# Performance work log

Hardware: AMD Instinct MI355X
Metric: run time of the kernel (lower is better)

Reference implementation:

```python
import jax, jax.numpy as jnp
import numpy as np

NUM_HEADS = 8
NUM_LAYERS = 6
NUM_POINTS = 25
# TrajParamIndex: X=0,Y=1,Z=2,VX=3,VY=4,AX=5,AY=6,YAW=7,LENGTH=8,WIDTH=9,HEIGHT=10


def _unit_cube_points(n=NUM_POINTS):
    m = int(np.sqrt(n))
    lin = np.linspace(-1.0, 1.0, m)
    pts = []
    for dim in range(3):
        for sign in (-1.0, 1.0):
            a, b = np.meshgrid(lin, lin, indexing='ij')
            s = np.full_like(a, sign)
            if dim == 0:
                p = np.stack([s, a, b], -1)
            elif dim == 1:
                p = np.stack([a, s, b], -1)
            else:
                p = np.stack([a, b, s], -1)
            pts.append(p.reshape(-1, 3))
    return jnp.asarray(np.concatenate(pts, 0), jnp.float32)  # [150,3]


def _ln(x, g, b):
    m = x.mean(-1, keepdims=True)
    v = ((x - m) ** 2).mean(-1, keepdims=True)
    return (x - m) / jnp.sqrt(v + 1e-5) * g + b


def _mha(q, k, v, wi, bi, wo, bo):
    E = q.shape[-1]
    d = E // NUM_HEADS
    qq = q @ wi[:E].T + bi[:E]
    kk = k @ wi[E:2 * E].T + bi[E:2 * E]
    vv = v @ wi[2 * E:].T + bi[2 * E:]
    B, S, _ = qq.shape
    Sk = kk.shape[1]
    qh = qq.reshape(B, S, NUM_HEADS, d)
    kh = kk.reshape(B, Sk, NUM_HEADS, d)
    vh = vv.reshape(B, Sk, NUM_HEADS, d)
    att = jnp.einsum('bqhd,bkhd->bhqk', qh, kh) / jnp.sqrt(jnp.float32(d))
    att = jax.nn.softmax(att, axis=-1)
    o = jnp.einsum('bhqk,bkhd->bqhd', att, vh).reshape(B, S, E)
    return o @ wo.T + bo


def _bilinear(feat, uv, valid):
    # feat [B,C,H,W], uv [B,M,2] in [0,1] (u along W), valid [B,M] -> [B,M,C]
    B, C, H, W = feat.shape
    px = uv[..., 0] * (W - 1)
    py = uv[..., 1] * (H - 1)
    x0 = jnp.floor(px)
    y0 = jnp.floor(py)
    wx = px - x0
    wy = py - y0
    x0i = jnp.clip(x0, 0, W - 1).astype(jnp.int32)
    x1i = jnp.clip(x0 + 1, 0, W - 1).astype(jnp.int32)
    y0i = jnp.clip(y0, 0, H - 1).astype(jnp.int32)
    y1i = jnp.clip(y0 + 1, 0, H - 1).astype(jnp.int32)
    flat = feat.reshape(B, C, H * W)
    take = jax.vmap(lambda f, i: f[:, i])  # [C,HW],[M] -> [C,M]
    f00 = take(flat, y0i * W + x0i)
    f01 = take(flat, y0i * W + x1i)
    f10 = take(flat, y1i * W + x0i)
    f11 = take(flat, y1i * W + x1i)
    wxb = wx[:, None, :]
    wyb = wy[:, None, :]
    out = (f00 * (1 - wxb) * (1 - wyb) + f01 * wxb * (1 - wyb)
           + f10 * (1 - wxb) * wyb + f11 * wxb * wyb)
    out = out * valid[:, None, :].astype(out.dtype)
    return out.transpose(0, 2, 1)


def _transform_points(box_pts, tp, ego_t, dt):
    # box_pts [B,N,P,3] local, tp [B,N,11], ego_t [B,4] (x,y,yaw,ts), dt [B]
    yaw = tp[..., 7][..., None]  # [B,N,1]
    c, s = jnp.cos(yaw), jnp.sin(yaw)
    lx, ly, lz = box_pts[..., 0], box_pts[..., 1], box_pts[..., 2]
    rx = lx * c - ly * s
    ry = lx * s + ly * c
    dtb = dt[:, None]  # [B,1]
    cx = tp[..., 0] + tp[..., 3] * dtb + 0.5 * tp[..., 5] * dtb ** 2  # [B,N]
    cy = tp[..., 1] + tp[..., 4] * dtb + 0.5 * tp[..., 6] * dtb ** 2
    cz = tp[..., 2]
    wx = rx + cx[..., None]
    wy = ry + cy[..., None]
    wz = lz + cz[..., None]
    ex = ego_t[:, 0][:, None, None]
    ey = ego_t[:, 1][:, None, None]
    eyaw = ego_t[:, 2][:, None, None]
    pxr = wx - ex
    pyr = wy - ey
    gx = pxr * jnp.cos(eyaw) + pyr * jnp.sin(eyaw)
    gy = -pxr * jnp.sin(eyaw) + pyr * jnp.cos(eyaw)
    return jnp.stack([gx, gy, wz], -1)


def _project(wp, cal):
    # wp [B,N,P,3], cal [B,8] = fx,fy,cx,cy,tx,ty,tz,cam_yaw -> uv in [0,1], valid
    fx, fy, cx0, cy0, tx, ty, tz, cyaw = [cal[:, i][:, None, None] for i in range(8)]
    px = wp[..., 0] - tx
    py = wp[..., 1] - ty
    pz = wp[..., 2] - tz
    fwd = px * jnp.cos(cyaw) + py * jnp.sin(cyaw)
    left = -px * jnp.sin(cyaw) + py * jnp.cos(cyaw)
    zc = fwd
    xc = -left
    yc = -pz
    vz = zc > 0.1
    zs = jnp.maximum(zc, 0.1)
    u = fx * xc / zs + cx0
    v = fy * yc / zs + cy0
    valid = vz & (u >= 0) & (u < 1) & (v >= 0) & (v < 1)
    return jnp.stack([u, v], -1), valid


def _forward(features, calib, ego_states, queries, query_pos,
             traj_w1, traj_b1, traj_w2, traj_b2,
             fm_w1, fm_b1, fm_w2, fm_b2,
             sa_in_w, sa_in_b, sa_out_w, sa_out_b,
             ca_in_w, ca_in_b, ca_out_w, ca_out_b,
             l1_w, l1_b, l2_w, l2_b,
             n1_g, n1_b, n2_g, n2_b, n3_g, n3_b):
    unit = _unit_cube_points()  # [P,3]
    P = unit.shape[0]
    cams, B, T = features.shape[0], features.shape[1], features.shape[2]
    Cf = features.shape[3]
    N = queries.shape[0]

    def traj_head(x):
        return jax.nn.relu(x @ traj_w1.T + traj_b1) @ traj_w2.T + traj_b2

    def feature_mlp(x):
        return jax.nn.relu(x @ fm_w1.T + fm_b1) @ fm_w2.T + fm_b2

    q = jnp.broadcast_to(queries[None], (B, N, queries.shape[1]))
    outputs = []
    for li in range(NUM_LAYERS):
        tp = traj_head(q)  # [B,N,11]
        outputs.append(tp)
        dims = tp[..., 8:11][:, :, None, :]  # [B,N,1,3] (L,W,H)
        box_pts = unit[None, None] * dims  # [B,N,P,3]
        acc = jnp.zeros((B, N, Cf), jnp.float32)
        for t in range(T):
            dt = ego_states[:, t, 3] - ego_states[:, -1, 3]  # [B]
            wp = _transform_points(box_pts, tp, ego_states[:, t], dt)
            for ci in range(cams):
                uv, valid = _project(wp, calib[ci])
                samp = _bilinear(features[ci, :, t], uv.reshape(B, N * P, 2),
                                 valid.reshape(B, N * P))  # [B,N*P,Cf]
                acc = acc + samp.reshape(B, N, P, Cf).sum(axis=2)
        agg = acc / jnp.float32(P * T * cams)
        mem = feature_mlp(agg)  # [B,N,Cf]
        # refine layer li (called without query_pos in decoder forward)
        sa = _mha(q, q, q, sa_in_w[li], sa_in_b[li], sa_out_w[li], sa_out_b[li])
        q = _ln(q + sa, n1_g[li], n1_b[li])
        ca = _mha(q, mem, mem, ca_in_w[li], ca_in_b[li], ca_out_w[li], ca_out_b[li])
        q = _ln(q + ca, n2_g[li], n2_b[li])
        ff = jax.nn.relu(q @ l1_w[li].T + l1_b[li]) @ l2_w[li].T + l2_b[li]
        q = _ln(q + ff, n3_g[li], n3_b[li])
    outputs.append(traj_head(q))
    return jnp.stack(outputs)  # [L+1,B,N,11]


def setup_inputs() -> dict:
    key = jax.random.key(0)
    ks = jax.random.split(key, 32)
    cams, B, T, Cf, H, W = 6, 1, 2, 256, 64, 160
    N, E, Dff, L = 128, 256, 512, NUM_LAYERS

    def rn(k, shape, scale=0.05):
        return jax.random.normal(k, shape, jnp.float32) * scale

    features = jax.random.normal(ks[0], (cams, B, T, Cf, H, W), jnp.float32)
    # calibration: fx,fy,cx,cy,tx,ty,tz,cam_yaw; cameras 8m behind origin along view dir
    cal = np.zeros((cams, B, 8), np.float32)
    for ci in range(cams):
        cyaw = ci * (2 * np.pi / cams)
        cal[ci, :, 0] = 1.2
        cal[ci, :, 1] = 1.6
        cal[ci, :, 2] = 0.5
        cal[ci, :, 3] = 0.5
        cal[ci, :, 4] = -8.0 * np.cos(cyaw)
        cal[ci, :, 5] = -8.0 * np.sin(cyaw)
        cal[ci, :, 6] = -0.5
        cal[ci, :, 7] = cyaw
    calib = jnp.asarray(cal)
    ego = np.zeros((B, T, 4), np.float32)
    for t in range(T):
        ego[:, t, 0] = 0.5 * t
        ego[:, t, 2] = 0.01 * t
        ego[:, t, 3] = 0.1 * t
    ego_states = jnp.asarray(ego)
    return {
        'features': features, 'calib': calib, 'ego_states': ego_states,
        'queries': rn(ks[1], (N, E), 1.0), 'query_pos': rn(ks[2], (N, E), 1.0),
        'traj_w1': rn(ks[3], (Dff, E)), 'traj_b1': jnp.zeros((Dff,), jnp.float32),
        'traj_w2': rn(ks[4], (11, Dff)), 'traj_b2': jnp.zeros((11,), jnp.float32),
        'fm_w1': rn(ks[5], (Dff, E)), 'fm_b1': jnp.zeros((Dff,), jnp.float32),
        'fm_w2': rn(ks[6], (E, Dff)), 'fm_b2': jnp.zeros((E,), jnp.float32),
        'sa_in_w': rn(ks[7], (L, 3 * E, E)), 'sa_in_b': jnp.zeros((L, 3 * E), jnp.float32),
        'sa_out_w': rn(ks[8], (L, E, E)), 'sa_out_b': jnp.zeros((L, E), jnp.float32),
        'ca_in_w': rn(ks[9], (L, 3 * E, E)), 'ca_in_b': jnp.zeros((L, 3 * E), jnp.float32),
        'ca_out_w': rn(ks[10], (L, E, E)), 'ca_out_b': jnp.zeros((L, E), jnp.float32),
        'l1_w': rn(ks[11], (L, Dff, E)), 'l1_b': jnp.zeros((L, Dff), jnp.float32),
        'l2_w': rn(ks[12], (L, E, Dff)), 'l2_b': jnp.zeros((L, E), jnp.float32),
        'n1_g': jnp.ones((L, E), jnp.float32), 'n1_b': jnp.zeros((L, E), jnp.float32),
        'n2_g': jnp.ones((L, E), jnp.float32), 'n2_b': jnp.zeros((L, E), jnp.float32),
        'n3_g': jnp.ones((L, E), jnp.float32), 'n3_b': jnp.zeros((L, E), jnp.float32),
    }


def reference(features, calib, ego_states, queries, query_pos,
              traj_w1, traj_b1, traj_w2, traj_b2,
              fm_w1, fm_b1, fm_w2, fm_b2,
              sa_in_w, sa_in_b, sa_out_w, sa_out_b,
              ca_in_w, ca_in_b, ca_out_w, ca_out_b,
              l1_w, l1_b, l2_w, l2_b,
              n1_g, n1_b, n2_g, n2_b, n3_g, n3_b):
    return _forward(features, calib, ego_states, queries, query_pos,
                    traj_w1, traj_b1, traj_w2, traj_b2,
                    fm_w1, fm_b1, fm_w2, fm_b2,
                    sa_in_w, sa_in_b, sa_out_w, sa_out_b,
                    ca_in_w, ca_in_b, ca_out_w, ca_out_b,
                    l1_w, l1_b, l2_w, l2_b,
                    n1_g, n1_b, n2_g, n2_b, n3_g, n3_b)
```

## Files before the change

kernel.cpp:

```cpp
#include <hip/hip_runtime.h>
#include <stdint.h>

typedef unsigned short u16;

#define DEV static __device__ __forceinline__

DEV float b2f(u16 u){ return __uint_as_float(((uint32_t)u) << 16); }
DEV u16 f2b(float f){ uint32_t x = __float_as_uint(f); return (u16)((x + 0x7fffu + ((x >> 16) & 1u)) >> 16); }
DEV int imin(int a, int b){ return a < b ? a : b; }
DEV int imax(int a, int b){ return a > b ? a : b; }

DEV int is_f32(const void* cal){
  float a = ((const float*)cal)[0];
  return (fabsf(a - 1.2f) < 1e-2f) ? 1 : 0;
}

DEV float ld(const void* p, size_t i, int f32){
  return f32 ? ((const float*)p)[i] : b2f(((const u16*)p)[i]);
}

__device__ float4 g_sawT[6*256*768/4];
__device__ float4 g_sowT[6*256*256/4];
__device__ float4 g_cawT[6*256*768/4];
__device__ float4 g_cowT[6*256*256/4];
__device__ float4 g_l1wT[6*256*512/4];
__device__ float4 g_l2wT[6*512*256/4];
__device__ float4 g_tw1T[256*512/4];
__device__ float4 g_fw1T[256*512/4];
__device__ float4 g_fw2T[512*256/4];

DEV float dotP(const float* x, const float4* wP, int col, const int N, const int K){
  const float4* p = wP + col;
  const float4* x4 = (const float4*)x;
  float s0=0.f,s1=0.f,s2=0.f,s3=0.f;
  #pragma unroll 8
  for(int k4 = 0; k4 < K/4; k4++){
    float4 w = p[(size_t)k4*N];
    float4 xv = x4[k4];
    s0 += xv.x*w.x; s1 += xv.y*w.y; s2 += xv.z*w.z; s3 += xv.w*w.w;
  }
  return (s0+s1)+(s2+s3);
}

DEV void dot2P(const float* x, const float4* wP, int c0, int c1, const int N,
               float* r0, float* r1){
  const float4* p0 = wP + c0;
  const float4* p1 = wP + c1;
  const float4* x4 = (const float4*)x;
  float a0=0,a1=0,a2=0,a3=0,b0=0,b1=0,b2=0,b3=0;
  #pragma unroll 8
  for(int k4 = 0; k4 < 64; k4++){
    float4 xv = x4[k4];
    float4 w0 = p0[(size_t)k4*N];
    float4 w1 = p1[(size_t)k4*N];
    a0+=xv.x*w0.x; a1+=xv.y*w0.y; a2+=xv.z*w0.z; a3+=xv.w*w0.w;
    b0+=xv.x*w1.x; b1+=xv.y*w1.y; b2+=xv.z*w1.z; b3+=xv.w*w1.w;
  }
  *r0=(a0+a1)+(a2+a3); *r1=(b0+b1)+(b2+b3);
}

DEV void dot3P(const float* x, const float4* wP, int t, float* r0, float* r1, float* r2){
  const float4* p0 = wP + t;
  const float4* p1 = wP + t + 256;
  const float4* p2 = wP + t + 512;
  const float4* x4 = (const float4*)x;
  float a0=0,a1=0,a2=0,a3=0,b0=0,b1=0,b2=0,b3=0,c0=0,c1=0,c2=0,c3=0;
  #pragma unroll 4
  for(int k4 = 0; k4 < 64; k4++){
    float4 xv = x4[k4];
    float4 w0 = p0[(size_t)k4*768];
    float4 w1 = p1[(size_t)k4*768];
    float4 w2 = p2[(size_t)k4*768];
    a0+=xv.x*w0.x; a1+=xv.y*w0.y; a2+=xv.z*w0.z; a3+=xv.w*w0.w;
    b0+=xv.x*w1.x; b1+=xv.y*w1.y; b2+=xv.z*w1.z; b3+=xv.w*w1.w;
    c0+=xv.x*w2.x; c1+=xv.y*w2.y; c2+=xv.z*w2.z; c3+=xv.w*w2.w;
  }
  *r0=(a0+a1)+(a2+a3); *r1=(b0+b1)+(b2+b3); *r2=(c0+c1)+(c2+c3);
}

DEV void kv_store_k(float* kT, int t, int qi, float val){
  int hh = t >> 5, i = t & 31;
  kT[((size_t)(hh*1024 + (i>>2)*128 + qi))*4 + (i&3)] = val;
}
DEV void kv_store_v(float* vP, int t, int qi, float val){
  vP[((size_t)((qi>>2)*256 + t))*4 + (qi&3)] = val;
}

DEV float attn_score(const float* qv, const float* kT, int hh, int k){
  const float4* kp = (const float4*)kT + hh*1024 + k;
  const float4* xq = (const float4*)(qv + hh*32);
  float s0=0.f, s1=0.f;
  #pragma unroll
  for(int i4 = 0; i4 < 8; i4 += 2){
    float4 w0 = kp[i4*128], w1 = kp[(i4+1)*128];
    float4 x0 = xq[i4],     x1 = xq[i4+1];
    s0 += x0.x*w0.x + x0.y*w0.y + x0.z*w0.z + x0.w*w0.w;
    s1 += x1.x*w1.x + x1.y*w1.y + x1.z*w1.z + x1.w*w1.w;
  }
  return s0+s1;
}

DEV float attn_av(const float* s, const float* vP, int hh, int t){
  const float4* vp = (const float4*)vP + t;
  const float4* sp = (const float4*)(s + hh*128);
  float a0=0.f, a1=0.f;
  #pragma unroll 8
  for(int k4 = 0; k4 < 32; k4 += 2){
    float4 w0 = vp[(size_t)k4*256], w1 = vp[(size_t)(k4+1)*256];
    float4 s0 = sp[k4],             s1 = sp[k4+1];
    a0 += s0.x*w0.x + s0.y*w0.y + s0.z*w0.z + s0.w*w0.w;
    a1 += s1.x*w1.x + s1.y*w1.y + s1.z*w1.z + s1.w*w1.w;
  }
  return a0+a1;
}

DEV float bsum256(float v, float* buf){
  int t = threadIdx.x;
  for(int off = 32; off > 0; off >>= 1) v += __shfl_xor(v, off);
  if((t & 63) == 0) buf[t >> 6] = v;
  __syncthreads();
  float r = buf[0] + buf[1] + buf[2] + buf[3];
  __syncthreads();
  return r;
}

DEV float lnorm(float r, const void* g, const void* b, size_t off, float* buf, int f32){
  float m = bsum256(r, buf) * (1.f/256.f);
  float d = r - m;
  float v = bsum256(d*d, buf) * (1.f/256.f);
  return d * rsqrtf(v + 1e-5f) * ld(g, off + threadIdx.x, f32) + ld(b, off + threadIdx.x, f32);
}

DEV void traj_headT(const float* qn, const void* b1, const void* w2, const void* b2,
                    float* hbuf, float* tp, void* out, int slot, int qi, int f32){
  int t = threadIdx.x;
  float h0, h1;
  dot2P(qn, g_tw1T, t, t + 256, 512, &h0, &h1);
  hbuf[t]     = fmaxf(0.f, ld(b1, t, f32)     + h0);
  hbuf[t+256] = fmaxf(0.f, ld(b1, t+256, f32) + h1);
  __syncthreads();
  if(t < 176){
    int o = t >> 4, lane = t & 15;
    float s = 0.f;
    for(int k = lane; k < 512; k += 16) s += hbuf[k] * ld(w2, o*512 + k, f32);
    for(int off = 8; off > 0; off >>= 1) s += __shfl_down(s, off, 16);
    if(lane == 0){
      s += ld(b2, o, f32);
      tp[qi*11 + o] = s;
      int oi = (slot*128 + qi)*11 + o;
      if(f32) ((float*)out)[oi] = s; else ((u16*)out)[oi] = f2b(s);
    }
  }
  __syncthreads();
}

DEV void softmax8(float* s){
  int t = threadIdx.x;
  int hh = t >> 5, lane = t & 31;
  float m = -1e30f;
  for(int k = lane; k < 128; k += 32) m = fmaxf(m, s[hh*128 + k]);
  for(int off = 16; off > 0; off >>= 1) m = fmaxf(m, __shfl_xor(m, off, 32));
  float ss = 0.f;
  for(int k = lane; k < 128; k += 32){
    float e = __expf(s[hh*128 + k] - m);
    s[hh*128 + k] = e; ss += e;
  }
  for(int off = 16; off > 0; off >>= 1) ss += __shfl_xor(ss, off, 32);
  float inv = 1.f / ss;
  for(int k = lane; k < 128; k += 32) s[hh*128 + k] *= inv;
}

__global__ __launch_bounds__(256) void k_wt(
    const void* saw, const void* sow, const void* caw, const void* cow,
    const void* l1w, const void* l2w, const void* tw1, const void* fw1, const void* fw2,
    const void* cal){
  int f32 = is_f32(cal);
  int t = threadIdx.x;
  __shared__ __align__(16) float tile[64*65];
  int bid = blockIdx.x;
  const void* src; float* dst; int N, K, NB, KB;
  if(bid < 288)      { src = saw; dst = (float*)g_sawT; N=768; K=256; NB=12; KB=4; }
  else if(bid < 384) { src = sow; dst = (float*)g_sowT; N=256; K=256; NB=4;  KB=4; bid -= 288; }
  else if(bid < 672) { src = caw; dst = (float*)g_cawT; N=768; K=256; NB=12; KB=4; bid -= 384; }
  else if(bid < 768) { src = cow; dst = (float*)g_cowT; N=256; K=256; NB=4;  KB=4; bid -= 672; }
  else if(bid < 960) { src = l1w; dst = (float*)g_l1wT; N=512; K=256; NB=8;  KB=4; bid -= 768; }
  else if(bid < 1152){ src = l2w; dst = (float*)g_l2wT; N=256; K=512; NB=4;  KB=8; bid -= 960; }
  else if(bid < 1184){ src = tw1; dst = (float*)g_tw1T; N=512; K=256; NB=8;  KB=4; bid -= 1152; }
  else if(bid < 1216){ src = fw1; dst = (float*)g_fw1T; N=512; K=256; NB=8;  KB=4; bid -= 1184; }
  else               { src = fw2; dst = (float*)g_fw2T; N=256; K=512; NB=4;  KB=8; bid -= 1216; }
  int nb = bid % NB;
  int kb = (bid / NB) % KB;
  int l  = bid / (NB*KB);
  for(int it = 0; it < 16; it++){
    int n = it*4 + (t >> 6);
    int k = t & 63;
    tile[n*65 + k] = ld(src, ((size_t)l*N + nb*64 + n)*K + kb*64 + k, f32);
  }
  __syncthreads();
  int kl = t & 3, nn = (t >> 2) & 15, wv = t >> 6;
  int n_local = wv*16 + nn;
  for(int k4 = 0; k4 < 16; k4++){
    int kcol = k4*4 + kl;
    size_t addr = (size_t)l*K*N + (((size_t)(kb*16 + k4))*N + nb*64 + n_local)*4 + kl;
    dst[addr] = tile[n_local*65 + kcol];
  }
}

__global__ __launch_bounds__(256) void k_trinit(const void* feat, u16* FTb, int use_ft,
    const void* queries, const void* tb1, const void* tw2, const void* tb2,
    const void* sab, const void* cal,
    float* q, float* tp, float* qrow, float* kTsa, float* vsa, float* acc, void* out){
  int f32 = is_f32(cal);
  int t = threadIdx.x;
  __shared__ __align__(16) u16 tile[64*258];
  if(blockIdx.x < 128){
    float* qn   = (float*)tile;
    float* hbuf = (float*)tile + 256;
    int qi = blockIdx.x;
    float v = ld(queries, qi*256 + t, f32);
    qn[t] = v; q[qi*256 + t] = v;
    __syncthreads();
    traj_headT(qn, tb1, tw2, tb2, hbuf, tp, out, 0, qi, f32);
    float c0, c1, c2;
    dot3P(qn, g_sawT, t, &c0, &c1, &c2);
    qrow[qi*256 + t] = ld(sab, t, f32)       + c0;
    kv_store_k(kTsa, t, qi, ld(sab, t + 256, f32) + c1);
    kv_store_v(vsa,  t, qi, ld(sab, t + 512, f32) + c2);
    acc[qi*256 + t] = 0.f;
    return;
  }
  if(!use_ft) return;
  int bid = blockIdx.x - 128;
  int pch = bid % 160; int e = bid / 160;
  if(f32){
    for(int it = 0; it < 64; it++){
      int ch = it*4 + (t >> 6);
      int p = t & 63;
      tile[p*258 + ch] = f2b(((const float*)feat)[((size_t)(e*256 + ch))*10240 + pch*64 + p]);
    }
  } else {
    for(int it = 0; it < 64; it++){
      int ch = it*4 + (t >> 6);
      int p = t & 63;
      tile[p*258 + ch] = ((const u16*)feat)[((size_t)(e*256 + ch))*10240 + pch*64 + p];
    }
  }
  __syncthreads();
  for(int it = 0; it < 16; it++){
    int p = it*4 + (t >> 6);
    int ch = (t & 63)*4;
    ushort4 v;
    v.x = tile[p*258 + ch];   v.y = tile[p*258 + ch+1];
    v.z = tile[p*258 + ch+2]; v.w = tile[p*258 + ch+3];
    *(ushort4*)&FTb[((size_t)(e*10240 + pch*64 + p))*256 + ch] = v;
  }
}

__global__ __launch_bounds__(256, 2) void k_samsa(const u16* FTb, const void* feat, int use_ft,
    const void* cal, const void* ego, const float* tp, float* acc,
    const float* q, const float* qrow, const float* kTsa, const float* vsa,
    const void* sob, const void* n1g, const void* n1b, const void* cab,
    int li, float* qs, float* qq){
  int t = threadIdx.x;
  int f32 = is_f32(cal);
  __shared__ __align__(16) float xa[256];
  __shared__ __align__(16) float s[1024];
  __shared__ __align__(16) float h[512];
  __shared__ float buf[8];
  __shared__ float tps[11];
  __shared__ int4  soff[152];
  __shared__ float4 sw[152];
  __shared__ float spx[152], spy[152];
  __shared__ int sval[152];
  __shared__ int plist[152];
  __shared__ int pcnt;

  if(blockIdx.x < 128){
    int qi = blockIdx.x;
    xa[t] = qrow[qi*256 + t];
    __syncthreads();
    for(int rep = 0; rep < 4; rep++){
      int idx = t + rep*256; int hh = idx >> 7, k = idx & 127;
      s[idx] = attn_score(xa, kTsa, hh, k) * 0.1767766952966369f;
    }
    __syncthreads();
    softmax8(s);
    __syncthreads();
    h[t] = attn_av(s, vsa, t >> 5, t);
    __syncthreads();
    float pr = ld(sob, (size_t)li*256 + t, f32) + dotP(h, g_sowT + (size_t)li*16384, t, 256, 256);
    float r = q[qi*256 + t] + pr;
    float y = lnorm(r, n1g, n1b, (size_t)li*256, buf, f32);
    qs[qi*256 + t] = y;
    __syncthreads();
    xa[t] = y;
    __syncthreads();
    qq[qi*256 + t] = ld(cab, (size_t)li*768 + t, f32)
                   + dotP(xa, g_cawT + (size_t)li*49152, t, 768, 256);
    return;
  }

  int sb = blockIdx.x - 128;
  int ob = (sb & 7) * 192 + (sb >> 3);
  int qi = ob & 127, e = ob >> 7;
  int ci = e >> 1, tt = e & 1;
  if(t == 0) pcnt = 0;
  if(t < 11) tps[t] = tp[qi*11 + t];
  __syncthreads();
  if(t < 150){
    float dt = ld(ego, tt*4 + 3, f32) - ld(ego, 7, f32);
    int face = t/25, rr = t%25, ii = rr/5, jj = rr%5;
    float av = -1.f + 0.5f*ii, bv = -1.f + 0.5f*jj;
    float sg = (face & 1) ? 1.f : -1.f; int dim = face >> 1;
    float ux = (dim == 0) ? sg : av;
    float uy = (dim == 0) ? av : ((dim == 1) ? sg : bv);
    float uz = (dim == 2) ? sg : bv;
    float lx = ux*tps[8], ly = uy*tps[9], lz = uz*tps[10];
    float yaw = tps[7];
    float cyw = cosf(yaw), syw = sinf(yaw);
    float rx = lx*cyw - ly*syw, ry = lx*syw + ly*cyw;
    float dt2 = 0.5f*dt*dt;
    float cxx = tps[0] + tps[3]*dt + tps[5]*dt2;
    float cyy = tps[1] + tps[4]*dt + tps[6]*dt2;
    float wx = rx + cxx, wy = ry + cyy, wz = lz + tps[2];
    float ex = ld(ego, tt*4, f32), ey = ld(ego, tt*4 + 1, f32), eyaw = ld(ego, tt*4 + 2, f32);
    float ce = cosf(eyaw), se = sinf(eyaw);
    float pxr = wx - ex, pyr = wy - ey;
    float gx = pxr*ce + pyr*se, gy = -pxr*se + pyr*ce;
    float fx = ld(cal, ci*8, f32),   fy = ld(cal, ci*8+1, f32);
    float cx0 = ld(cal, ci*8+2, f32), cy0 = ld(cal, ci*8+3, f32);
    float tx = ld(cal, ci*8+4, f32), ty = ld(cal, ci*8+5, f32);
    float tz = ld(cal, ci*8+6, f32), cw = ld(cal, ci*8+7, f32);
    float cc = cosf(cw), sc = sinf(cw);
    float pxc = gx - tx, pyc = gy - ty, pzc = wz - tz;
    float zc = pxc*cc + pyc*sc;
    float left = -pxc*sc + pyc*cc;
    float xc = -left, yc = -pzc;
    float zs = fmaxf(zc, 0.1f);
    float u = fx*xc/zs + cx0, vv = fy*yc/zs + cy0;
    bool val = (zc > 0.1f) && (u >= 0.f) && (u < 1.f) && (vv >= 0.f) && (vv < 1.f);
    float px = u*159.f, py = vv*63.f;
    spx[t] = px; spy[t] = py;
    float x0f = floorf(px), y0f = floorf(py);
    float wxf = px - x0f, wyf = py - y0f;
    int x0 = imin(imax((int)x0f, 0), 159), y0 = imin(imax((int)y0f, 0), 63);
    int x1 = imin(x0 + 1, 159), y1 = imin(y0 + 1, 63);
    soff[t] = make_int4((y0*160 + x0)*128, (y0*160 + x1)*128,
                        (y1*160 + x0)*128, (y1*160 + x1)*128);
    sw[t] = make_float4((1.f-wxf)*(1.f-wyf), wxf*(1.f-wyf), (1.f-wxf)*wyf, wxf*wyf);
    sval[t] = val ? 1 : 0;
    if(val){ int ix = atomicAdd(&pcnt, 1); plist[ix] = t; }
  }
  __syncthreads();
  if(use_ft){
    int c2 = (t & 127) * 2;
    int half = t >> 7;
    const uint32_t* base = (const uint32_t*)FTb + (size_t)e*10240*128 + (c2 >> 1);
    int np = pcnt;
    int split = (np + 1) >> 1;
    int lo = half ? split : 0;
    int hi = half ? np : split;
    float a0 = 0.f, a1 = 0.f;
    int pp = lo;
    for(; pp + 2 <= hi; pp += 2){
      int p0 = plist[pp], p1 = plist[pp+1];
      int4 o0 = soff[p0]; int4 o1 = soff[p1];
      float4 w0 = sw[p0]; float4 w1 = sw[p1];
      uint32_t u00 = base[o0.x], u01 = base[o0.y], u02 = base[o0.z], u03 = base[o0.w];
      uint32_t u10 = base[o1.x], u11 = base[o1.y], u12 = base[o1.z], u13 = base[o1.w];
      a0 += w0.x*__uint_as_float(u00<<16) + w0.y*__uint_as_float(u01<<16)
          + w0.z*__uint_as_float(u02<<16) + w0.w*__uint_as_float(u03<<16);
      a1 += w0.x*__uint_as_float(u00&0xffff0000u) + w0.y*__uint_as_float(u01&0xffff0000u)
          + w0.z*__uint_as_float(u02&0xffff0000u) + w0.w*__uint_as_float(u03&0xffff0000u);
      a0 += w1.x*__uint_as_float(u10<<16) + w1.y*__uint_as_float(u11<<16)
          + w1.z*__uint_as_float(u12<<16) + w1.w*__uint_as_float(u13<<16);
      a1 += w1.x*__uint_as_float(u10&0xffff0000u) + w1.y*__uint_as_float(u11&0xffff0000u)
          + w1.z*__uint_as_float(u12&0xffff0000u) + w1.w*__uint_as_float(u13&0xffff0000u);
    }
    for(; pp < hi; pp++){
      int p = plist[pp];
      int4 o = soff[p]; float4 w = sw[p];
      uint32_t u0 = base[o.x], u1 = base[o.y], u2 = base[o.z], u3 = base[o.w];
      a0 += w.x*__uint_as_float(u0<<16) + w.y*__uint_as_float(u1<<16)
          + w.z*__uint_as_float(u2<<16) + w.w*__uint_as_float(u3<<16);
      a1 += w.x*__uint_as_float(u0&0xffff0000u) + w.y*__uint_as_float(u1&0xffff0000u)
          + w.z*__uint_as_float(u2&0xffff0000u) + w.w*__uint_as_float(u3&0xffff0000u);
    }
    s[half*256 + c2]     = a0;
    s[half*256 + c2 + 1] = a1;
    __syncthreads();
    atomicAdd(&acc[qi*256 + t], s[t] + s[256 + t]);
  } else {
    float a = 0.f;
    size_t pc = ((size_t)e*256 + t)*10240;
    for(int p = 0; p < 150; p++){
      if(!sval[p]) continue;
      float px = spx[p], py = spy[p];
      float x0f = floorf(px), y0f = floorf(py);
      float wxf = px - x0f, wyf = py - y0f;
      int x0 = imin(imax((int)x0f, 0), 159), y0 = imin(imax((int)y0f, 0), 63);
      int x1 = imin(x0 + 1, 159), y1 = imin(y0 + 1, 63);
      float w00 = (1.f-wxf)*(1.f-wyf), w01 = wxf*(1.f-wyf), w10 = (1.f-wxf)*wyf, w11 = wxf*wyf;
      a += w00*ld(feat, pc + y0*160 + x0, f32) + w01*ld(feat, pc + y0*160 + x1, f32)
         + w10*ld(feat, pc + y1*160 + x0, f32) + w11*ld(feat, pc + y1*160 + x1, f32);
    }
    atomicAdd(&acc[qi*256 + t], a);
  }
}

__global__ __launch_bounds__(256, 2) void k_mk(const float* acc,
    const void* fb1, const void* fb2, const void* cab, const void* cal,
    int li, float* kvK, float* kvV){
  __shared__ __align__(16) float xa[256];
  __shared__ __align__(16) float h[512];
  int t = threadIdx.x, qi = blockIdx.x;
  int f32 = is_f32(cal);
  xa[t] = acc[qi*256 + t] * (1.f/1800.f);
  __syncthreads();
  float h0, h1;
  dot2P(xa, g_fw1T, t, t + 256, 512, &h0, &h1);
  h[t]     = fmaxf(0.f, ld(fb1, t, f32)     + h0);
  h[t+256] = fmaxf(0.f, ld(fb1, t+256, f32) + h1);
  __syncthreads();
  float m = ld(fb2, t, f32) + dotP(h, g_fw2T, t, 256, 512);
  __syncthreads();
  xa[t] = m;
  __syncthreads();
  const float4* cawT = g_cawT + (size_t)li*49152;
  float kk, vv;
  dot2P(xa, cawT, 256 + t, 512 + t, 768, &kk, &vv);
  size_t bo = (size_t)li*768;
  kv_store_k(kvK, t, qi, ld(cab, bo + 256 + t, f32) + kk);
  kv_store_v(kvV, t, qi, ld(cab, bo + 512 + t, f32) + vv);
}

__global__ __launch_bounds__(256, 2) void k_ca(const float* qs, const float* qq,
    const float* kvK, const float* kvV,
    const void* cob, const void* n2g, const void* n2b,
    const void* l1b, const void* l2b, const void* n3g, const void* n3b,
    const void* tb1, const void* tw2, const void* tb2, const void* sab, const void* cal,
    int li, int have_next,
    float* qout, float* qrow, float* kTsa, float* vsa,
    float* tp, float* acc, void* out){
  __shared__ __align__(16) float qv[256]; __shared__ __align__(16) float s[1024];
  __shared__ __align__(16) float o[256];  __shared__ __align__(16) float q2[256];
  __shared__ __align__(16) float h[512];  __shared__ float buf[8];
  int t = threadIdx.x, qi = blockIdx.x;
  int f32 = is_f32(cal);
  qv[t] = qq[qi*256 + t];
  __syncthreads();
  for(int rep = 0; rep < 4; rep++){
    int idx = t + rep*256; int hh = idx >> 7, k = idx & 127;
    s[idx] = attn_score(qv, kvK, hh, k) * 0.1767766952966369f;
  }
  __syncthreads();
  softmax8(s);
  __syncthreads();
  o[t] = attn_av(s, kvV, t >> 5, t);
  __syncthreads();
  float pr = ld(cob, (size_t)li*256 + t, f32) + dotP(o, g_cowT + (size_t)li*16384, t, 256, 256);
  float r = qs[qi*256 + t] + pr;
  float y = lnorm(r, n2g, n2b, (size_t)li*256, buf, f32);
  q2[t] = y;
  __syncthreads();
  float h0, h1;
  dot2P(q2, g_l1wT + (size_t)li*32768, t, t + 256, 512, &h0, &h1);
  h[t]     = fmaxf(0.f, ld(l1b, (size_t)li*512 + t, f32)     + h0);
  h[t+256] = fmaxf(0.f, ld(l1b, (size_t)li*512 + t+256, f32) + h1);
  __syncthreads();
  float ff = ld(l2b, (size_t)li*256 + t, f32) + dotP(h, g_l2wT + (size_t)li*32768, t, 256, 512);
  float r3 = q2[t] + ff;
  float y3 = lnorm(r3, n3g, n3b, (size_t)li*256, buf, f32);
  qout[qi*256 + t] = y3;
  __syncthreads();
  q2[t] = y3;
  __syncthreads();
  traj_headT(q2, tb1, tw2, tb2, h, tp, out, li + 1, qi, f32);
  if(have_next){
    float c0, c1, c2;
    dot3P(q2, g_sawT + (size_t)(li+1)*49152, t, &c0, &c1, &c2);
    size_t sb = (size_t)(li+1)*768;
    qrow[qi*256 + t] = ld(sab, sb + t, f32) + c0;
    kv_store_k(kTsa, t, qi, ld(sab, sb + 256 + t, f32) + c1);
    kv_store_v(vsa,  t, qi, ld(sab, sb + 512 + t, f32) + c2);
  }
  acc[qi*256 + t] = 0.f;
}

extern "C" void kernel_launch(void* const* d_in, const int* in_sizes, int n_in,
                              void* d_out, int out_size, void* d_ws, size_t ws_size,
                              hipStream_t stream){
  const void* feat    = d_in[0];
  const void* calib   = d_in[1];
  const void* ego     = d_in[2];
  const void* queries = d_in[3];
  const void* tw1 = d_in[5];  const void* tb1 = d_in[6];
  const void* tw2 = d_in[7];  const void* tb2 = d_in[8];
  const void* fw1 = d_in[9];  const void* fb1 = d_in[10];
  const void* fw2 = d_in[11]; const void* fb2 = d_in[12];
  const void* saw = d_in[13]; const void* sab = d_in[14];
  const void* sow = d_in[15]; const void* sob = d_in[16];
  const void* caw = d_in[17]; const void* cab = d_in[18];
  const void* cow = d_in[19]; const void* cob = d_in[20];
  const void* l1w = d_in[21]; const void* l1b = d_in[22];
  const void* l2w = d_in[23]; const void* l2b = d_in[24];
  const void* n1g = d_in[25]; const void* n1b = d_in[26];
  const void* n2g = d_in[27]; const void* n2b = d_in[28];
  const void* n3g = d_in[29]; const void* n3b = d_in[30];

  float* ws   = (float*)d_ws;
  float* q    = ws + 16;
  float* qs   = ws + 32784;
  float* tp   = ws + 65552;
  float* qrow = ws + 67088;
  float* kTsa = ws + 99856;
  float* vsa  = ws + 132624;
  float* kvK  = ws + 165392;
  float* kvV  = ws + 198160;
  float* qq   = ws + 230928;
  float* acc  = ws + 263696;
  u16*   FTb  = (u16*)(ws + 296464);
  size_t need = (size_t)296464*4 + (size_t)12*10240*256*2;
  int use_ft = (ws_size >= need) ? 1 : 0;

  k_wt<<<1248, 256, 0, stream>>>(saw, sow, caw, cow, l1w, l2w, tw1, fw1, fw2, calib);
  k_trinit<<<2048, 256, 0, stream>>>(feat, FTb, use_ft,
                                     queries, tb1, tw2, tb2, sab, calib,
                                     q, tp, qrow, kTsa, vsa, acc, d_out);
  for(int li = 0; li < 6; li++){
    k_samsa<<<1664, 256, 0, stream>>>(FTb, feat, use_ft, calib, ego, tp, acc,
                                      q, qrow, kTsa, vsa, sob, n1g, n1b, cab,
                                      li, qs, qq);
    k_mk<<<128, 256, 0, stream>>>(acc, fb1, fb2, cab, calib, li, kvK, kvV);
    int hn = (li < 5) ? 1 : 0;
    k_ca<<<128, 256, 0, stream>>>(qs, qq, kvK, kvV, cob, n2g, n2b,
                                  l1b, l2b, n3g, n3b,
                                  tb1, tw2, tb2, sab, calib, li, hn,
                                  q, qrow, kTsa, vsa, tp, acc, d_out);
  }
  (void)in_sizes; (void)n_in; (void)out_size;
}
```

Measured before the change: 942.8 us.

## Fuse feature-MLP and cross-attn K/V projection into sampling kernel via last-block counter

Removes the separate k_mk launch per layer. Each of the twelve sampling blocks per query bumps an atomic counter after adding into acc, and the last block to finish runs the feature MLP and the cross-attention K/V projection for that query. Counters are reset in the init kernel and in k_ca. This saves six kernel launches and their gaps, but it adds fences and atomics, puts the MLP tail on whichever block finishes last, and the fused kernel needs more shared memory and registers, which can lower occupancy.

```diff
diff --git a/kernel.cpp b/kernel.cpp
--- a/kernel.cpp
+++ b/kernel.cpp
@@ -209,7 +209,8 @@
 __global__ __launch_bounds__(256) void k_trinit(const void* feat, u16* FTb, int use_ft,
     const void* queries, const void* tb1, const void* tw2, const void* tb2,
     const void* sab, const void* cal,
-    float* q, float* tp, float* qrow, float* kTsa, float* vsa, float* acc, void* out){
+    float* q, float* tp, float* qrow, float* kTsa, float* vsa, float* acc,
+    int* dcnt, void* out){
   int f32 = is_f32(cal);
   int t = threadIdx.x;
   __shared__ __align__(16) u16 tile[64*258];
@@ -217,6 +218,7 @@
     float* qn   = (float*)tile;
     float* hbuf = (float*)tile + 256;
     int qi = blockIdx.x;
+    if(t == 0) dcnt[qi] = 0;
     float v = ld(queries, qi*256 + t, f32);
     qn[t] = v; q[qi*256 + t] = v;
     __syncthreads();
@@ -260,7 +262,8 @@
     const void* cal, const void* ego, const float* tp, float* acc,
     const float* q, const float* qrow, const float* kTsa, const float* vsa,
     const void* sob, const void* n1g, const void* n1b, const void* cab,
-    int li, float* qs, float* qq){
+    const void* fb1, const void* fb2,
+    int li, float* qs, float* qq, float* kvK, float* kvV, int* dcnt){
   int t = threadIdx.x;
   int f32 = is_f32(cal);
   __shared__ __align__(16) float xa[256];
@@ -274,6 +277,7 @@
   __shared__ int sval[152];
   __shared__ int plist[152];
   __shared__ int pcnt;
+  __shared__ int last_flag;
 
   if(blockIdx.x < 128){
     int qi = blockIdx.x;
@@ -406,29 +410,32 @@
     }
     atomicAdd(&acc[qi*256 + t], a);
   }
-}
-
-__global__ __launch_bounds__(256, 2) void k_mk(const float* acc,
-    const void* fb1, const void* fb2, const void* cab, const void* cal,
-    int li, float* kvK, float* kvV){
-  __shared__ __align__(16) float xa[256];
-  __shared__ __align__(16) float h[512];
-  int t = threadIdx.x, qi = blockIdx.x;
-  int f32 = is_f32(cal);
-  xa[t] = acc[qi*256 + t] * (1.f/1800.f);
+
+  __threadfence();
+  __syncthreads();
+  if(t == 0){
+    int old = atomicAdd(&dcnt[qi], 1);
+    last_flag = (old == 11) ? 1 : 0;
+  }
+  __syncthreads();
+  if(!last_flag) return;
+  __threadfence();
+  float* mx = s;
+  float* mh = s + 256;
+  mx[t] = acc[qi*256 + t] * (1.f/1800.f);
   __syncthreads();
   float h0, h1;
-  dot2P(xa, g_fw1T, t, t + 256, 512, &h0, &h1);
-  h[t]     = fmaxf(0.f, ld(fb1, t, f32)     + h0);
-  h[t+256] = fmaxf(0.f, ld(fb1, t+256, f32) + h1);
-  __syncthreads();
-  float m = ld(fb2, t, f32) + dotP(h, g_fw2T, t, 256, 512);
-  __syncthreads();
-  xa[t] = m;
+  dot2P(mx, g_fw1T, t, t + 256, 512, &h0, &h1);
+  mh[t]     = fmaxf(0.f, ld(fb1, t, f32)     + h0);
+  mh[t+256] = fmaxf(0.f, ld(fb1, t+256, f32) + h1);
+  __syncthreads();
+  float m = ld(fb2, t, f32) + dotP(mh, g_fw2T, t, 256, 512);
+  __syncthreads();
+  mx[t] = m;
   __syncthreads();
   const float4* cawT = g_cawT + (size_t)li*49152;
   float kk, vv;
-  dot2P(xa, cawT, 256 + t, 512 + t, 768, &kk, &vv);
+  dot2P(mx, cawT, 256 + t, 512 + t, 768, &kk, &vv);
   size_t bo = (size_t)li*768;
   kv_store_k(kvK, t, qi, ld(cab, bo + 256 + t, f32) + kk);
   kv_store_v(kvV, t, qi, ld(cab, bo + 512 + t, f32) + vv);
@@ -441,12 +448,13 @@
     const void* tb1, const void* tw2, const void* tb2, const void* sab, const void* cal,
     int li, int have_next,
     float* qout, float* qrow, float* kTsa, float* vsa,
-    float* tp, float* acc, void* out){
+    float* tp, float* acc, int* dcnt, void* out){
   __shared__ __align__(16) float qv[256]; __shared__ __align__(16) float s[1024];
   __shared__ __align__(16) float o[256];  __shared__ __align__(16) float q2[256];
   __shared__ __align__(16) float h[512];  __shared__ float buf[8];
   int t = threadIdx.x, qi = blockIdx.x;
   int f32 = is_f32(cal);
+  if(t == 0) dcnt[qi] = 0;
   qv[t] = qq[qi*256 + t];
   __syncthreads();
   for(int rep = 0; rep < 4; rep++){
@@ -512,6 +520,7 @@
   float* q    = ws + 16;
   float* qs   = ws + 32784;
   float* tp   = ws + 65552;
+  int*   dcnt = (int*)(ws + 66960);
   float* qrow = ws + 67088;
   float* kTsa = ws + 99856;
   float* vsa  = ws + 132624;
@@ -526,17 +535,16 @@
   k_wt<<<1248, 256, 0, stream>>>(saw, sow, caw, cow, l1w, l2w, tw1, fw1, fw2, calib);
   k_trinit<<<2048, 256, 0, stream>>>(feat, FTb, use_ft,
                                      queries, tb1, tw2, tb2, sab, calib,
-                                     q, tp, qrow, kTsa, vsa, acc, d_out);
+                                     q, tp, qrow, kTsa, vsa, acc, dcnt, d_out);
   for(int li = 0; li < 6; li++){
     k_samsa<<<1664, 256, 0, stream>>>(FTb, feat, use_ft, calib, ego, tp, acc,
                                       q, qrow, kTsa, vsa, sob, n1g, n1b, cab,
-                                      li, qs, qq);
-    k_mk<<<128, 256, 0, stream>>>(acc, fb1, fb2, cab, calib, li, kvK, kvV);
+                                      fb1, fb2, li, qs, qq, kvK, kvV, dcnt);
     int hn = (li < 5) ? 1 : 0;
     k_ca<<<128, 256, 0, stream>>>(qs, qq, kvK, kvV, cob, n2g, n2b,
                                   l1b, l2b, n3g, n3b,
                                   tb1, tw2, tb2, sab, calib, li, hn,
-                                  q, qrow, kTsa, vsa, tp, acc, d_out);
+                                  q, qrow, kTsa, vsa, tp, acc, dcnt, d_out);
   }
   (void)in_sizes; (void)n_in; (void)out_size;
 }
```

Result: slower. 1.851 ms (+96.3%).
